# Kernel tuning notes

Hardware: AMD Instinct MI355X
Metric: run time of the kernel (lower is better)

Reference implementation:

```python
import jax, jax.numpy as jnp
import numpy as np

N_NODES = 50000
N_EDGES = 1000000
NEG_SLOPE = 0.2


def _gat_layer(x, W, attn_l, attn_r, bias, src, dst, n_nodes):
    """DGL-style GATConv. x:[N,Fin], W:[H*D,Fin], attn_l/attn_r:[H,D], bias:[H*D].
    Returns [N, H*D] after ReLU activation (flattened heads)."""
    H, D = attn_l.shape
    h = (x @ W.T).reshape(n_nodes, H, D)                    # [N,H,D]
    el = jnp.sum(h * attn_l[None], axis=-1)                 # [N,H]
    er = jnp.sum(h * attn_r[None], axis=-1)                 # [N,H]
    e = jax.nn.leaky_relu(el[src] + er[dst], NEG_SLOPE)     # [E,H]
    # edge softmax over incoming edges per destination node
    emax = jax.ops.segment_max(e, dst, num_segments=n_nodes)  # [N,H]
    emax = jnp.where(jnp.isfinite(emax), emax, 0.0)
    a = jnp.exp(e - emax[dst])                               # [E,H]
    denom = jax.ops.segment_sum(a, dst, num_segments=n_nodes)  # [N,H]
    alpha = a / denom[dst]                                   # [E,H]
    msg = alpha[:, :, None] * h[src]                         # [E,H,D]
    out = jax.ops.segment_sum(msg, dst, num_segments=n_nodes)  # [N,H,D]
    out = out + bias.reshape(1, H, D)
    out = jax.nn.relu(out)
    return out.reshape(n_nodes, H * D)


def setup_inputs() -> dict:
    key = jax.random.key(0)
    ks = jax.random.split(key, 16)
    features = jax.random.normal(ks[0], (N_NODES, 25), dtype=jnp.float32)
    src = jax.random.randint(ks[1], (N_EDGES,), 0, N_NODES, dtype=jnp.int32)
    dst = jax.random.randint(ks[2], (N_EDGES,), 0, N_NODES, dtype=jnp.int32)

    def glorot(k, shape, fan):
        return jax.random.normal(k, shape, dtype=jnp.float32) * (1.0 / np.sqrt(fan))

    # layer 1: in=25, out=10, heads=4
    W1 = glorot(ks[3], (40, 25), 25)
    al1 = glorot(ks[4], (4, 10), 10)
    ar1 = glorot(ks[5], (4, 10), 10)
    b1 = jnp.zeros((40,), dtype=jnp.float32)
    # layer 2: in=40, out=25, heads=4
    W2 = glorot(ks[6], (100, 40), 40)
    al2 = glorot(ks[7], (4, 25), 25)
    ar2 = glorot(ks[8], (4, 25), 25)
    b2 = jnp.zeros((100,), dtype=jnp.float32)
    # layer 3: in=100, out=50, heads=1
    W3 = glorot(ks[9], (50, 100), 100)
    al3 = glorot(ks[10], (1, 50), 50)
    ar3 = glorot(ks[11], (1, 50), 50)
    b3 = jnp.zeros((50,), dtype=jnp.float32)
    # final fc: 50 -> 93
    fc_w = glorot(ks[12], (93, 50), 50)
    fc_b = jnp.zeros((93,), dtype=jnp.float32)
    return {
        "features": features, "src": src, "dst": dst,
        "W1": W1, "al1": al1, "ar1": ar1, "b1": b1,
        "W2": W2, "al2": al2, "ar2": ar2, "b2": b2,
        "W3": W3, "al3": al3, "ar3": ar3, "b3": b3,
        "fc_w": fc_w, "fc_b": fc_b,
    }


def reference(features, src, dst,
              W1, al1, ar1, b1,
              W2, al2, ar2, b2,
              W3, al3, ar3, b3,
              fc_w, fc_b):
    n = features.shape[0]
    h = _gat_layer(features, W1, al1, ar1, b1, src, dst, n)   # [N,40]
    h = _gat_layer(h, W2, al2, ar2, b2, src, dst, n)          # [N,100]
    h = _gat_layer(h, W3, al3, ar3, b3, src, dst, n)          # [N,50]
    return h @ fc_w.T + fc_b                                  # [N,93]
```

## Files before the change

kernel.cpp:

```cpp
#include <hip/hip_runtime.h>
#include <hip/hip_bf16.h>

#ifndef NEG_SLOPE
#define NEG_SLOPE 0.2f
#endif

static inline int cdiv(long long a, long long b) { return (int)((a + b - 1) / b); }

__device__ __forceinline__ float lrelu(float v) { return v > 0.f ? v : NEG_SLOPE * v; }

__global__ void k_build_wext(const float* __restrict__ W1, const float* __restrict__ al1,
                             const float* __restrict__ ar1, const float* __restrict__ W2,
                             const float* __restrict__ al2, const float* __restrict__ ar2,
                             const float* __restrict__ W3, const float* __restrict__ al3,
                             const float* __restrict__ ar3, float* __restrict__ wx1,
                             float* __restrict__ wx2, float* __restrict__ wx3) {
    int b = blockIdx.x;
    const float *W, *al, *ar;
    float* wx;
    int FIN, FOUT, H, D;
    if (b == 0) { W = W1; al = al1; ar = ar1; wx = wx1; FIN = 25; FOUT = 40; H = 4; D = 10; }
    else if (b == 1) { W = W2; al = al2; ar = ar2; wx = wx2; FIN = 40; FOUT = 100; H = 4; D = 25; }
    else { W = W3; al = al3; ar = ar3; wx = wx3; FIN = 100; FOUT = 50; H = 1; D = 50; }
    for (int i = threadIdx.x; i < FOUT * FIN; i += blockDim.x) wx[i] = W[i];
    for (int i = threadIdx.x; i < 2 * H * FIN; i += blockDim.x) {
        int row = i / FIN, k = i % FIN;
        int h = row % H, isR = row / H;
        const float* a = isR ? ar : al;
        float s = 0.f;
        for (int d = 0; d < D; ++d) s += W[(h * D + d) * FIN + k] * a[h * D + d];
        wx[(FOUT + isR * H + h) * FIN + k] = s;
    }
}

template <int FIN, int FOUT, int H>
__global__ void k_linear(const float* __restrict__ x, const float* __restrict__ wx,
                         float* __restrict__ h, float* __restrict__ el, float* __restrict__ er,
                         int n_nodes) {
    constexpr int FOUTE = FOUT + 2 * H;
    __shared__ float Ws[FIN * FOUTE];
    for (int i = threadIdx.x; i < FIN * FOUTE; i += blockDim.x) {
        int f = i / FIN, k = i % FIN;
        Ws[k * FOUTE + f] = wx[i];
    }
    __syncthreads();
    int idx = blockIdx.x * blockDim.x + threadIdx.x;
    if (idx >= n_nodes * FOUTE) return;
    int n = idx / FOUTE, f = idx % FOUTE;
    const float* __restrict__ xr = x + (long long)n * FIN;
    float acc = 0.f;
#pragma unroll
    for (int k = 0; k < FIN; ++k) acc += xr[k] * Ws[k * FOUTE + f];
    if (f < FOUT) h[(long long)n * FOUT + f] = acc;
    else if (f < FOUT + H) el[n * H + (f - FOUT)] = acc;
    else er[n * H + (f - FOUT - H)] = acc;
}

__global__ void k_deg(const int* __restrict__ dst, int* __restrict__ deg, int n_edges) {
    int e = blockIdx.x * blockDim.x + threadIdx.x;
    if (e >= n_edges) return;
    atomicAdd(&deg[dst[e]], 1);
}

__global__ void k_scan_block(const int* __restrict__ deg, int* __restrict__ incl,
                             int* __restrict__ blocksum, int n) {
    __shared__ int tmp[256];
    int t = threadIdx.x;
    int i = blockIdx.x * 256 + t;
    int v = (i < n) ? deg[i] : 0;
    tmp[t] = v;
    __syncthreads();
    for (int off = 1; off < 256; off <<= 1) {
        int add = (t >= off) ? tmp[t - off] : 0;
        __syncthreads();
        tmp[t] += add;
        __syncthreads();
    }
    if (i < n) incl[i] = tmp[t];
    if (t == 255) blocksum[blockIdx.x] = tmp[t];
}

__global__ void k_scan_top(const int* __restrict__ blocksum, int* __restrict__ blockoff, int nb) {
    __shared__ int tmp[256];
    int t = threadIdx.x;
    int base = 0;
    for (int c = 0; c < nb; c += 256) {
        int i = c + t;
        int v = (i < nb) ? blocksum[i] : 0;
        tmp[t] = v;
        __syncthreads();
        for (int off = 1; off < 256; off <<= 1) {
            int add = (t >= off) ? tmp[t - off] : 0;
            __syncthreads();
            tmp[t] += add;
            __syncthreads();
        }
        if (i < nb) blockoff[i] = base + tmp[t] - v;
        base += tmp[255];
        __syncthreads();
    }
}

__global__ void k_scan_finalize(const int* __restrict__ incl, const int* __restrict__ deg,
                                const int* __restrict__ blockoff, int* __restrict__ rowptr,
                                int n, int n_edges) {
    int i = blockIdx.x * blockDim.x + threadIdx.x;
    if (i < n) rowptr[i] = incl[i] - deg[i] + blockoff[i / 256];
    if (i == 0) rowptr[n] = n_edges;
}

__global__ void k_fill(const int* __restrict__ src, const int* __restrict__ dst,
                       const int* __restrict__ rowptr, int* __restrict__ cursor,
                       int* __restrict__ csr_src, int n_edges) {
    int e = blockIdx.x * blockDim.x + threadIdx.x;
    if (e >= n_edges) return;
    int d = dst[e];
    int pos = atomicAdd(&cursor[d], 1);
    csr_src[rowptr[d] + pos] = src[e];
}

__global__ void k_sort_wave(const int* __restrict__ rowptr, int* __restrict__ csr_src,
                            int n_nodes) {
    int wid = (blockIdx.x * blockDim.x + threadIdx.x) >> 6;
    int lane = threadIdx.x & 63;
    if (wid >= n_nodes) return;
    int s0 = rowptr[wid], e0 = rowptr[wid + 1];
    int d = e0 - s0;
    if (d <= 1) return;
    if (d <= 64) {
        int v = (lane < d) ? csr_src[s0 + lane] : 0x7FFFFFFF;
        int rank = 0;
        for (int k = 0; k < d; ++k) {
            int vk = __shfl(v, k);
            rank += (vk < v || (vk == v && k < lane)) ? 1 : 0;
        }
        if (lane < d) csr_src[s0 + rank] = v;
    } else if (lane == 0) {
        for (int a = s0 + 1; a < e0; ++a) {
            int key = csr_src[a];
            int b = a - 1;
            while (b >= s0 && csr_src[b] > key) { csr_src[b + 1] = csr_src[b]; --b; }
            csr_src[b + 1] = key;
        }
    }
}

template <int FOUT, int H, int D, int EB>
__global__ __launch_bounds__(256, 4) void k_node_gather(
    const int* __restrict__ rowptr, const int* __restrict__ csr_src,
    const float* __restrict__ el, const float* __restrict__ er, const float* __restrict__ h,
    const float* __restrict__ bias, float* __restrict__ xout, int n_nodes) {
    constexpr int P = FOUT / 2;
    constexpr int NP = (EB * H + 63) / 64;
    int wid = (blockIdx.x * blockDim.x + threadIdx.x) >> 6;
    int lane = threadIdx.x & 63;
    if (wid >= n_nodes) return;
    int start = rowptr[wid], end = rowptr[wid + 1];

    const int hh_p = lane % H;
    const float er_c = er[wid * H + hh_p];
    const int f0 = 2 * lane, f1 = 2 * lane + 1;
    const int hh0 = (lane < P) ? f0 / D : 0;
    const int hh1 = (lane < P) ? f1 / D : 0;
    float acc0 = 0.f, acc1 = 0.f, den_acc = 0.f;

    if (start < end) {
        int j0 = start;
        int nb = end - j0;
        if (nb > EB) nb = EB;
        int s_c[NP];
        float e_c[NP];
#pragma unroll
        for (int q = 0; q < NP; ++q) {
            int ei = (q * 64 + lane) / H;
            s_c[q] = csr_src[j0 + (ei < nb ? ei : 0)];
            e_c[q] = el[s_c[q] * H + hh_p];
        }
        while (true) {
            int j1 = j0 + nb;
            int nbn = end - j1;
            if (nbn > EB) nbn = EB;
            int s_n[NP];
            float e_n[NP];
            if (nbn > 0) {
#pragma unroll
                for (int q = 0; q < NP; ++q) {
                    int ei = (q * 64 + lane) / H;
                    s_n[q] = csr_src[j1 + (ei < nbn ? ei : 0)];
                    e_n[q] = el[s_n[q] * H + hh_p];
                }
            }
            float p_c[NP];
#pragma unroll
            for (int q = 0; q < NP; ++q) p_c[q] = expf(lrelu(e_c[q] + er_c));
            float pd = 0.f;
#pragma unroll
            for (int q = 0; q < NP; ++q) {
                int ei = (q * 64 + lane) / H;
                pd += (ei < nb) ? p_c[q] : 0.f;
            }
#pragma unroll
            for (int st = H; st < 64; st <<= 1) pd += __shfl_xor(pd, st);
            den_acc += pd;
            float2 hv[EB];
#pragma unroll
            for (int e = 0; e < EB; ++e) {
                if (e < nb) {
                    int sreg = __shfl(s_c[(e * H) >> 6], (e * H) & 63);
                    if (lane < P)
                        hv[e] = ((const float2*)(h + (long long)sreg * FOUT))[lane];
                }
            }
#pragma unroll
            for (int e = 0; e < EB; ++e) {
                if (e < nb) {
                    float p0 = __shfl(p_c[(e * H) >> 6], ((e * H) & 63) + hh0);
                    float p1 = __shfl(p_c[(e * H) >> 6], ((e * H) & 63) + hh1);
                    if (lane < P) {
                        acc0 += p0 * hv[e].x;
                        acc1 += p1 * hv[e].y;
                    }
                }
            }
            if (nbn <= 0) break;
            j0 = j1;
            nb = nbn;
#pragma unroll
            for (int q = 0; q < NP; ++q) {
                s_c[q] = s_n[q];
                e_c[q] = e_n[q];
            }
        }
    }
    if (lane < P) {
        float d0 = __shfl(den_acc, hh0);
        float d1 = __shfl(den_acc, hh1);
        float b0 = bias[f0], b1 = bias[f1];
        float v0, v1;
        if (end > start) { v0 = acc0 / d0 + b0; v1 = acc1 / d1 + b1; }
        else { v0 = b0; v1 = b1; }
        float2 o;
        o.x = v0 > 0.f ? v0 : 0.f;
        o.y = v1 > 0.f ? v1 : 0.f;
        ((float2*)(xout + (long long)wid * FOUT))[lane] = o;
    }
}

template <int FIN, int FOUT>
__global__ void k_fc(const float* __restrict__ x, const float* __restrict__ W,
                     const float* __restrict__ b, float* __restrict__ out, int n_nodes) {
    __shared__ float Ws[FIN * FOUT];
    for (int i = threadIdx.x; i < FIN * FOUT; i += blockDim.x) {
        int f = i / FIN, k = i % FIN;
        Ws[k * FOUT + f] = W[i];
    }
    __syncthreads();
    int idx = blockIdx.x * blockDim.x + threadIdx.x;
    if (idx >= n_nodes * FOUT) return;
    int n = idx / FOUT, f = idx % FOUT;
    const float* __restrict__ xr = x + (long long)n * FIN;
    float acc = b[f];
#pragma unroll
    for (int k = 0; k < FIN; ++k) acc += xr[k] * Ws[k * FOUT + f];
    out[idx] = acc;
}

template <int FIN, int FOUT, int H, int D, int EB>
static void gat_layer(const float* x, const float* wext, const float* bias, const int* rowptr,
                      const int* csr_src, int n_nodes, float* bufH, float* el, float* er,
                      float* xnext, hipStream_t stream) {
    constexpr int FOUTE = FOUT + 2 * H;
    k_linear<FIN, FOUT, H><<<cdiv((long long)n_nodes * FOUTE, 256), 256, 0, stream>>>(
        x, wext, bufH, el, er, n_nodes);
    k_node_gather<FOUT, H, D, EB><<<cdiv((long long)n_nodes * 64, 256), 256, 0, stream>>>(
        rowptr, csr_src, el, er, bufH, bias, xnext, n_nodes);
}

extern "C" void kernel_launch(void* const* d_in, const int* in_sizes, int n_in,
                              void* d_out, int out_size, void* d_ws, size_t ws_size,
                              hipStream_t stream) {
    const float* features = (const float*)d_in[0];
    const int* src = (const int*)d_in[1];
    const int* dst = (const int*)d_in[2];
    const float* W1 = (const float*)d_in[3];
    const float* al1 = (const float*)d_in[4];
    const float* ar1 = (const float*)d_in[5];
    const float* b1 = (const float*)d_in[6];
    const float* W2 = (const float*)d_in[7];
    const float* al2 = (const float*)d_in[8];
    const float* ar2 = (const float*)d_in[9];
    const float* b2 = (const float*)d_in[10];
    const float* W3 = (const float*)d_in[11];
    const float* al3 = (const float*)d_in[12];
    const float* ar3 = (const float*)d_in[13];
    const float* b3 = (const float*)d_in[14];
    const float* fc_w = (const float*)d_in[15];
    const float* fc_b = (const float*)d_in[16];

    const int n_nodes = in_sizes[0] / 25;
    const int n_edges = in_sizes[1];
    const int nblocks_nodes = cdiv(n_nodes, 256);

    char* ws = (char*)d_ws;
    size_t off = 0;
    auto alloc = [&](size_t bytes) {
        char* p = ws + off;
        off += (bytes + 255) & ~(size_t)255;
        return p;
    };
    float* bufA = (float*)alloc((size_t)n_nodes * 100 * sizeof(float));
    float* bufH = (float*)alloc((size_t)n_nodes * 100 * sizeof(float));
    float* el = (float*)alloc((size_t)n_nodes * 4 * sizeof(float));
    float* er = (float*)alloc((size_t)n_nodes * 4 * sizeof(float));
    int* degcur = (int*)alloc((size_t)2 * n_nodes * sizeof(int));
    int* deg = degcur;
    int* cursor = degcur + n_nodes;
    int* incl = (int*)alloc((size_t)n_nodes * sizeof(int));
    int* blocksum = (int*)alloc((size_t)nblocks_nodes * sizeof(int));
    int* blockoff = (int*)alloc((size_t)nblocks_nodes * sizeof(int));
    int* rowptr = (int*)alloc((size_t)(n_nodes + 1) * sizeof(int));
    int* csr_src = (int*)alloc((size_t)n_edges * sizeof(int));
    float* wx1 = (float*)alloc((size_t)48 * 25 * sizeof(float));
    float* wx2 = (float*)alloc((size_t)108 * 40 * sizeof(float));
    float* wx3 = (float*)alloc((size_t)52 * 100 * sizeof(float));
    (void)ws_size;

    k_build_wext<<<3, 256, 0, stream>>>(W1, al1, ar1, W2, al2, ar2, W3, al3, ar3, wx1, wx2, wx3);

    hipMemsetAsync(degcur, 0, (size_t)2 * n_nodes * sizeof(int), stream);
    k_deg<<<cdiv(n_edges, 256), 256, 0, stream>>>(dst, deg, n_edges);
    k_scan_block<<<nblocks_nodes, 256, 0, stream>>>(deg, incl, blocksum, n_nodes);
    k_scan_top<<<1, 256, 0, stream>>>(blocksum, blockoff, nblocks_nodes);
    k_scan_finalize<<<cdiv(n_nodes + 1, 256), 256, 0, stream>>>(incl, deg, blockoff, rowptr,
                                                                n_nodes, n_edges);
    k_fill<<<cdiv(n_edges, 256), 256, 0, stream>>>(src, dst, rowptr, cursor, csr_src, n_edges);
    k_sort_wave<<<cdiv((long long)n_nodes * 64, 256), 256, 0, stream>>>(rowptr, csr_src,
                                                                        n_nodes);

    gat_layer<25, 40, 4, 10, 32>(features, wx1, b1, rowptr, csr_src, n_nodes, bufH, el, er,
                                 bufA, stream);
    gat_layer<40, 100, 4, 25, 32>(bufA, wx2, b2, rowptr, csr_src, n_nodes, bufH, el, er,
                                  bufA, stream);
    gat_layer<100, 50, 1, 50, 32>(bufA, wx3, b3, rowptr, csr_src, n_nodes, bufH, el, er,
                                  bufA, stream);

    k_fc<50, 93><<<cdiv((long long)n_nodes * 93, 256), 256, 0, stream>>>(
        bufA, fc_w, fc_b, (float*)d_out, n_nodes);
}
```

Baseline: 547.3 us.

## Restructure node gather with vector-width rows and double-buffered edge sub-batches

The per-destination gather kernel no longer loads up to 32 neighbor rows into registers at once. It processes edges in sub-batches of 4 with two register buffers, so the next sub-batch's row loads are issued while the current one is accumulated. Each lane now handles a templated vector width (float4 for the 4-head layers, float2 for the single-head layer). Edges per batch are sized so one wave covers a batch's attention logits with one register per lane. The aim is lower register pressure and higher occupancy without losing memory-level parallelism, at the cost of fewer loads in flight per wave and dropping the explicit launch bounds.

```diff
diff --git a/kernel.cpp b/kernel.cpp
--- a/kernel.cpp
+++ b/kernel.cpp
@@ -8,6 +8,28 @@
 static inline int cdiv(long long a, long long b) { return (int)((a + b - 1) / b); }
 
 __device__ __forceinline__ float lrelu(float v) { return v > 0.f ? v : NEG_SLOPE * v; }
+
+template <int VW> struct VecIO;
+template <> struct VecIO<2> {
+    static __device__ __forceinline__ void load(const float* p, int lane, float* o) {
+        float2 t = ((const float2*)p)[lane];
+        o[0] = t.x; o[1] = t.y;
+    }
+    static __device__ __forceinline__ void store(float* p, int lane, const float* v) {
+        float2 t; t.x = v[0]; t.y = v[1];
+        ((float2*)p)[lane] = t;
+    }
+};
+template <> struct VecIO<4> {
+    static __device__ __forceinline__ void load(const float* p, int lane, float* o) {
+        float4 t = ((const float4*)p)[lane];
+        o[0] = t.x; o[1] = t.y; o[2] = t.z; o[3] = t.w;
+    }
+    static __device__ __forceinline__ void store(float* p, int lane, const float* v) {
+        float4 t; t.x = v[0]; t.y = v[1]; t.z = v[2]; t.w = v[3];
+        ((float4*)p)[lane] = t;
+    }
+};
 
 __global__ void k_build_wext(const float* __restrict__ W1, const float* __restrict__ al1,
                              const float* __restrict__ ar1, const float* __restrict__ W2,
@@ -145,104 +167,121 @@
     }
 }
 
-template <int FOUT, int H, int D, int EB>
-__global__ __launch_bounds__(256, 4) void k_node_gather(
-    const int* __restrict__ rowptr, const int* __restrict__ csr_src,
-    const float* __restrict__ el, const float* __restrict__ er, const float* __restrict__ h,
-    const float* __restrict__ bias, float* __restrict__ xout, int n_nodes) {
-    constexpr int P = FOUT / 2;
-    constexpr int NP = (EB * H + 63) / 64;
+template <int FOUT, int H, int D, int VW>
+__global__ void k_node_gather(const int* __restrict__ rowptr, const int* __restrict__ csr_src,
+                              const float* __restrict__ el, const float* __restrict__ er,
+                              const float* __restrict__ h, const float* __restrict__ bias,
+                              float* __restrict__ xout, int n_nodes) {
+    constexpr int P = FOUT / VW;
+    constexpr int EB = (H == 1) ? 32 : (64 / H);
+    constexpr int SB = 4;
+    constexpr int NSB = EB / SB;
     int wid = (blockIdx.x * blockDim.x + threadIdx.x) >> 6;
     int lane = threadIdx.x & 63;
     if (wid >= n_nodes) return;
     int start = rowptr[wid], end = rowptr[wid + 1];
 
     const int hh_p = lane % H;
+    const int eidx = lane / H;
     const float er_c = er[wid * H + hh_p];
-    const int f0 = 2 * lane, f1 = 2 * lane + 1;
-    const int hh0 = (lane < P) ? f0 / D : 0;
-    const int hh1 = (lane < P) ? f1 / D : 0;
-    float acc0 = 0.f, acc1 = 0.f, den_acc = 0.f;
+    const bool isF = lane < P;
+
+    int hhA = 0, hhB = 0;
+    bool useB[VW];
+#pragma unroll
+    for (int c = 0; c < VW; ++c) useB[c] = false;
+    if (isF) {
+        hhA = (VW * lane) / D;
+        hhB = (VW * lane + VW - 1) / D;
+#pragma unroll
+        for (int c = 0; c < VW; ++c) useB[c] = ((VW * lane + c) / D) != hhA;
+    }
+
+    float acc[VW];
+#pragma unroll
+    for (int c = 0; c < VW; ++c) acc[c] = 0.f;
+    float den_acc = 0.f;
 
     if (start < end) {
         int j0 = start;
         int nb = end - j0;
         if (nb > EB) nb = EB;
-        int s_c[NP];
-        float e_c[NP];
-#pragma unroll
-        for (int q = 0; q < NP; ++q) {
-            int ei = (q * 64 + lane) / H;
-            s_c[q] = csr_src[j0 + (ei < nb ? ei : 0)];
-            e_c[q] = el[s_c[q] * H + hh_p];
-        }
+        int s_c = csr_src[j0 + (eidx < nb ? eidx : 0)];
+        float e_c = el[s_c * H + hh_p];
+        float p_c = 0.f;
+
+        auto loadsub = [&](int k, float (&buf)[SB][VW]) {
+#pragma unroll
+            for (int e2 = 0; e2 < SB; ++e2) {
+                int ge = k * SB + e2;
+                int sreg = __shfl(s_c, ge * H);
+                if (ge < nb && isF) VecIO<VW>::load(h + (long long)sreg * FOUT, lane, buf[e2]);
+            }
+        };
+        auto consume = [&](int k, float (&buf)[SB][VW]) {
+#pragma unroll
+            for (int e2 = 0; e2 < SB; ++e2) {
+                int ge = k * SB + e2;
+                float pA = __shfl(p_c, ge * H + hhA);
+                float pB = __shfl(p_c, ge * H + hhB);
+                if (ge < nb && isF) {
+#pragma unroll
+                    for (int c = 0; c < VW; ++c) acc[c] += (useB[c] ? pB : pA) * buf[e2][c];
+                }
+            }
+        };
+
         while (true) {
             int j1 = j0 + nb;
             int nbn = end - j1;
             if (nbn > EB) nbn = EB;
-            int s_n[NP];
-            float e_n[NP];
+            int s_n = 0;
+            float e_n = 0.f;
             if (nbn > 0) {
-#pragma unroll
-                for (int q = 0; q < NP; ++q) {
-                    int ei = (q * 64 + lane) / H;
-                    s_n[q] = csr_src[j1 + (ei < nbn ? ei : 0)];
-                    e_n[q] = el[s_n[q] * H + hh_p];
-                }
+                s_n = csr_src[j1 + (eidx < nbn ? eidx : 0)];
+                e_n = el[s_n * H + hh_p];
             }
-            float p_c[NP];
-#pragma unroll
-            for (int q = 0; q < NP; ++q) p_c[q] = expf(lrelu(e_c[q] + er_c));
-            float pd = 0.f;
-#pragma unroll
-            for (int q = 0; q < NP; ++q) {
-                int ei = (q * 64 + lane) / H;
-                pd += (ei < nb) ? p_c[q] : 0.f;
-            }
+
+            float hvA[SB][VW], hvB[SB][VW];
+            loadsub(0, hvA);
+
+            p_c = expf(lrelu(e_c + er_c));
+            float pd = (eidx < nb) ? p_c : 0.f;
 #pragma unroll
             for (int st = H; st < 64; st <<= 1) pd += __shfl_xor(pd, st);
             den_acc += pd;
-            float2 hv[EB];
-#pragma unroll
-            for (int e = 0; e < EB; ++e) {
-                if (e < nb) {
-                    int sreg = __shfl(s_c[(e * H) >> 6], (e * H) & 63);
-                    if (lane < P)
-                        hv[e] = ((const float2*)(h + (long long)sreg * FOUT))[lane];
+
+#pragma unroll
+            for (int sb = 0; sb < NSB; ++sb) {
+                if (sb + 1 < NSB) {
+                    if (sb & 1) loadsub(sb + 1, hvA);
+                    else loadsub(sb + 1, hvB);
                 }
+                if (sb & 1) consume(sb, hvB);
+                else consume(sb, hvA);
             }
-#pragma unroll
-            for (int e = 0; e < EB; ++e) {
-                if (e < nb) {
-                    float p0 = __shfl(p_c[(e * H) >> 6], ((e * H) & 63) + hh0);
-                    float p1 = __shfl(p_c[(e * H) >> 6], ((e * H) & 63) + hh1);
-                    if (lane < P) {
-                        acc0 += p0 * hv[e].x;
-                        acc1 += p1 * hv[e].y;
-                    }
-                }
-            }
+
             if (nbn <= 0) break;
             j0 = j1;
             nb = nbn;
-#pragma unroll
-            for (int q = 0; q < NP; ++q) {
-                s_c[q] = s_n[q];
-                e_c[q] = e_n[q];
-            }
-        }
-    }
-    if (lane < P) {
-        float d0 = __shfl(den_acc, hh0);
-        float d1 = __shfl(den_acc, hh1);
-        float b0 = bias[f0], b1 = bias[f1];
-        float v0, v1;
-        if (end > start) { v0 = acc0 / d0 + b0; v1 = acc1 / d1 + b1; }
-        else { v0 = b0; v1 = b1; }
-        float2 o;
-        o.x = v0 > 0.f ? v0 : 0.f;
-        o.y = v1 > 0.f ? v1 : 0.f;
-        ((float2*)(xout + (long long)wid * FOUT))[lane] = o;
+            s_c = s_n;
+            e_c = e_n;
+        }
+    }
+
+    float dA = __shfl(den_acc, hhA);
+    float dB = __shfl(den_acc, hhB);
+    if (isF) {
+        float bvals[VW], o[VW];
+        VecIO<VW>::load(bias, lane, bvals);
+#pragma unroll
+        for (int c = 0; c < VW; ++c) {
+            float v;
+            if (end > start) v = acc[c] / (useB[c] ? dB : dA) + bvals[c];
+            else v = bvals[c];
+            o[c] = v > 0.f ? v : 0.f;
+        }
+        VecIO<VW>::store(xout + (long long)wid * FOUT, lane, o);
     }
 }
 
@@ -265,14 +304,14 @@
     out[idx] = acc;
 }
 
-template <int FIN, int FOUT, int H, int D, int EB>
+template <int FIN, int FOUT, int H, int D, int VW>
 static void gat_layer(const float* x, const float* wext, const float* bias, const int* rowptr,
                       const int* csr_src, int n_nodes, float* bufH, float* el, float* er,
                       float* xnext, hipStream_t stream) {
     constexpr int FOUTE = FOUT + 2 * H;
     k_linear<FIN, FOUT, H><<<cdiv((long long)n_nodes * FOUTE, 256), 256, 0, stream>>>(
         x, wext, bufH, el, er, n_nodes);
-    k_node_gather<FOUT, H, D, EB><<<cdiv((long long)n_nodes * 64, 256), 256, 0, stream>>>(
+    k_node_gather<FOUT, H, D, VW><<<cdiv((long long)n_nodes * 64, 256), 256, 0, stream>>>(
         rowptr, csr_src, el, er, bufH, bias, xnext, n_nodes);
 }
 
@@ -337,12 +376,12 @@
     k_sort_wave<<<cdiv((long long)n_nodes * 64, 256), 256, 0, stream>>>(rowptr, csr_src,
                                                                         n_nodes);
 
-    gat_layer<25, 40, 4, 10, 32>(features, wx1, b1, rowptr, csr_src, n_nodes, bufH, el, er,
+    gat_layer<25, 40, 4, 10, 4>(features, wx1, b1, rowptr, csr_src, n_nodes, bufH, el, er,
+                                bufA, stream);
+    gat_layer<40, 100, 4, 25, 4>(bufA, wx2, b2, rowptr, csr_src, n_nodes, bufH, el, er,
                                  bufA, stream);
-    gat_layer<40, 100, 4, 25, 32>(bufA, wx2, b2, rowptr, csr_src, n_nodes, bufH, el, er,
-                                  bufA, stream);
-    gat_layer<100, 50, 1, 50, 32>(bufA, wx3, b3, rowptr, csr_src, n_nodes, bufH, el, er,
-                                  bufA, stream);
+    gat_layer<100, 50, 1, 50, 2>(bufA, wx3, b3, rowptr, csr_src, n_nodes, bufH, el, er,
+                                 bufA, stream);
 
     k_fc<50, 93><<<cdiv((long long)n_nodes * 93, 256), 256, 0, stream>>>(
         bufA, fc_w, fc_b, (float*)d_out, n_nodes);
```

After: 1.193 ms. +118.1%, slower.
